# Performance work log

Hardware: AMD Instinct MI355X
Metric: run time of the kernel (lower is better)

The kernel has to match this reference:

```python
import jax, jax.numpy as jnp
import numpy as np

N = 8192  # number of DAG nodes


def setup_inputs() -> dict:
    key = jax.random.key(0)
    k1, k2, k3 = jax.random.split(key, 3)
    thresholds = jax.random.normal(k1, (N,), dtype=jnp.float32)
    # children in [-1, N): -1 marks a leaf (no child)
    left = jax.random.randint(k2, (N,), -1, N, dtype=jnp.int32)
    right = jax.random.randint(k3, (N,), -1, N, dtype=jnp.int32)
    return {"thresholds": thresholds, "left": left, "right": right}


def reference(thresholds, left, right):
    # BFS fixed-point reachability from node 0, N sequential relaxation steps.
    n_nodes = left.shape[0]

    def step(reachable, _):
        # route children of reachable non-leaf nodes into a scatter; dump
        # inactive slots into the sentinel index n_nodes (dropped on slice)
        active_left = jnp.where(reachable & (left >= 0), left, n_nodes)
        active_right = jnp.where(reachable & (right >= 0), right, n_nodes)
        new_reachable = jnp.zeros(n_nodes + 1, dtype=jnp.bool_)
        new_reachable = new_reachable.at[active_left].set(True)
        new_reachable = new_reachable.at[active_right].set(True)
        new_reachable = new_reachable.at[0].set(True)
        return (new_reachable[:n_nodes] | reachable, None)

    init = jnp.zeros(n_nodes, dtype=jnp.bool_).at[0].set(True)
    mask, _ = jax.lax.scan(step, init, None, length=n_nodes)
    return mask
```

## Files before the change

kernel.cpp:

```cpp
#include <hip/hip_runtime.h>


#define NMAX 8192
#define BLK  256

__global__ __launch_bounds__(BLK) void dag_reach_kernel(
    const int* __restrict__ left,
    const int* __restrict__ right,
    int* __restrict__ out,
    int n)
{
    __shared__ int2         sLR[NMAX];
    __shared__ unsigned int visited[NMAX / 32];
    __shared__ int          frontier[NMAX];
    __shared__ int          s_qcount;

    const int tid = threadIdx.x;

    {
        const int4* l4 = (const int4*)left;
        const int4* r4 = (const int4*)right;
        const int nv = n / 4;
        for (int i = tid; i < nv; i += BLK) {
            int4 l = l4[i];
            int4 r = r4[i];
            int b = i * 4;
            sLR[b + 0] = make_int2(l.x, r.x);
            sLR[b + 1] = make_int2(l.y, r.y);
            sLR[b + 2] = make_int2(l.z, r.z);
            sLR[b + 3] = make_int2(l.w, r.w);
        }
    }
    for (int i = tid; i < NMAX / 32; i += BLK) visited[i] = 0u;
    if (tid == 0) { visited[0] = 1u; frontier[0] = 0; s_qcount = 1; }
    __syncthreads();

    int start = 0, end = 1;
    while (start < end) {
        for (int i = start + tid; i < end; i += BLK) {
            int node = frontier[i];
            int2 lr = sLR[node];
            if (lr.x >= 0) {
                unsigned int bit = 1u << (lr.x & 31);
                unsigned int old = atomicOr(&visited[lr.x >> 5], bit);
                if (!(old & bit))
                    frontier[atomicAdd(&s_qcount, 1)] = lr.x;
            }
            if (lr.y >= 0) {
                unsigned int bit = 1u << (lr.y & 31);
                unsigned int old = atomicOr(&visited[lr.y >> 5], bit);
                if (!(old & bit))
                    frontier[atomicAdd(&s_qcount, 1)] = lr.y;
            }
        }
        __syncthreads();
        start = end;
        end = s_qcount;
        __syncthreads();
    }

    {
        int4* o4 = (int4*)out;
        const int nv = n / 4;
        for (int i = tid; i < nv; i += BLK) {
            unsigned int w = visited[i >> 3];
            int sh = (i & 7) * 4;
            o4[i] = make_int4((int)((w >> (sh + 0)) & 1u),
                              (int)((w >> (sh + 1)) & 1u),
                              (int)((w >> (sh + 2)) & 1u),
                              (int)((w >> (sh + 3)) & 1u));
        }
    }
}

extern "C" void kernel_launch(void* const* d_in, const int* in_sizes, int n_in,
                              void* d_out, int out_size, void* d_ws, size_t ws_size,
                              hipStream_t stream)
{
    const int* left  = (const int*)d_in[1];
    const int* right = (const int*)d_in[2];
    int* out = (int*)d_out;
    const int n = in_sizes[1];

    dag_reach_kernel<<<1, BLK, 0, stream>>>(left, right, out, n);
}
```

Before: 74.42 us.

## Replace level-synchronous BFS with asynchronous work-queue traversal

Replaces the per-level BFS loop, which needs two block-wide barriers per level, with an asynchronous shared-memory work queue. Each of 256 worker threads claims a queue slot, spins until a node is written there, expands its children and claims the next slot. Termination is detected when the count of processed nodes equals the count of reserved slots. The block grows to 1024 threads for loading and output while only 256 do the traversal. This removes the barrier cost on long, narrow BFS chains, but it adds volatile polling, extra atomics, and a risk of spin or livelock behaviour across wavefronts.

After: 77.52 us. 4.2% more time.

```diff
diff --git a/kernel.cpp b/kernel.cpp
--- a/kernel.cpp
+++ b/kernel.cpp
@@ -1,8 +1,9 @@
 #include <hip/hip_runtime.h>
 
 
-#define NMAX 8192
-#define BLK  256
+#define NMAX  8192
+#define BLK   1024
+#define NWORK 256
 
 __global__ __launch_bounds__(BLK) void dag_reach_kernel(
     const int* __restrict__ left,
@@ -12,15 +13,15 @@
 {
     __shared__ int2         sLR[NMAX];
     __shared__ unsigned int visited[NMAX / 32];
-    __shared__ int          frontier[NMAX];
-    __shared__ int          s_qcount;
+    __shared__ int          queue[NMAX];
+    __shared__ int          s_tail, s_res, s_done;
 
     const int tid = threadIdx.x;
+    const int nv = n / 4;
 
     {
         const int4* l4 = (const int4*)left;
         const int4* r4 = (const int4*)right;
-        const int nv = n / 4;
         for (int i = tid; i < nv; i += BLK) {
             int4 l = l4[i];
             int4 r = r4[i];
@@ -31,37 +32,57 @@
             sLR[b + 3] = make_int2(l.w, r.w);
         }
     }
+    for (int i = tid; i < NMAX; i += BLK) queue[i] = -1;
     for (int i = tid; i < NMAX / 32; i += BLK) visited[i] = 0u;
-    if (tid == 0) { visited[0] = 1u; frontier[0] = 0; s_qcount = 1; }
+    if (tid == 0) { s_tail = 0; s_res = 1; s_done = 0; queue[0] = 0; visited[0] = 1u; }
     __syncthreads();
 
-    int start = 0, end = 1;
-    while (start < end) {
-        for (int i = start + tid; i < end; i += BLK) {
-            int node = frontier[i];
-            int2 lr = sLR[node];
-            if (lr.x >= 0) {
-                unsigned int bit = 1u << (lr.x & 31);
-                unsigned int old = atomicOr(&visited[lr.x >> 5], bit);
-                if (!(old & bit))
-                    frontier[atomicAdd(&s_qcount, 1)] = lr.x;
-            }
-            if (lr.y >= 0) {
-                unsigned int bit = 1u << (lr.y & 31);
-                unsigned int old = atomicOr(&visited[lr.y >> 5], bit);
-                if (!(old & bit))
-                    frontier[atomicAdd(&s_qcount, 1)] = lr.y;
+    if (tid < NWORK) {
+        volatile int* vq    = queue;
+        volatile int* vdone = &s_done;
+        volatile int* vres  = &s_res;
+
+        int myidx = atomicAdd(&s_tail, 1);
+        int node  = -1;
+
+        for (;;) {
+            if (node < 0 && myidx < NMAX) node = vq[myidx];
+            bool ready = (node >= 0);
+            if (__any(ready)) {
+                if (ready) {
+                    int2 lr = sLR[node];
+                    if (lr.x >= 0) {
+                        unsigned int bit = 1u << (lr.x & 31);
+                        unsigned int old = atomicOr(&visited[lr.x >> 5], bit);
+                        if (!(old & bit)) {
+                            int s = atomicAdd(&s_res, 1);
+                            queue[s] = lr.x;
+                        }
+                    }
+                    if (lr.y >= 0) {
+                        unsigned int bit = 1u << (lr.y & 31);
+                        unsigned int old = atomicOr(&visited[lr.y >> 5], bit);
+                        if (!(old & bit)) {
+                            int s = atomicAdd(&s_res, 1);
+                            queue[s] = lr.y;
+                        }
+                    }
+                    __threadfence_block();
+                    atomicAdd(&s_done, 1);
+                    myidx = atomicAdd(&s_tail, 1);
+                    node  = -1;
+                }
+            } else {
+                int d = *vdone;
+                int r = *vres;
+                if (d == r) break;
             }
         }
-        __syncthreads();
-        start = end;
-        end = s_qcount;
-        __syncthreads();
     }
+    __syncthreads();
 
     {
         int4* o4 = (int4*)out;
-        const int nv = n / 4;
         for (int i = tid; i < nv; i += BLK) {
             unsigned int w = visited[i >> 3];
             int sh = (i & 7) * 4;
```

## Replace level-synchronous BFS queue with asynchronous bitmap-owner propagation

Applied to the files above, without the earlier changes.

The frontier queue and per-level barriers are replaced by an owner-computes scheme. Each of 1024 threads owns 8 nodes and spins on a volatile read of the shared visited bitmap, expanding newly set bits with atomicOr. Convergence is found by quiescence counters and then a verification pass with block barriers, which avoids one barrier pair per BFS level along long chains. The risks are wasted spinning, heavy atomic contention on shared words, and correctness that depends on the quiescence heuristic plus the verify loop.

New measurement: 72.32 us. 2.8% less time.

```diff
diff --git a/kernel.cpp b/kernel.cpp
--- a/kernel.cpp
+++ b/kernel.cpp
@@ -2,7 +2,7 @@
 
 
 #define NMAX 8192
-#define BLK  256
+#define BLK  1024
 
 __global__ __launch_bounds__(BLK) void dag_reach_kernel(
     const int* __restrict__ left,
@@ -12,15 +12,14 @@
 {
     __shared__ int2         sLR[NMAX];
     __shared__ unsigned int visited[NMAX / 32];
-    __shared__ int          frontier[NMAX];
-    __shared__ int          s_qcount;
+    __shared__ int          flag[2];
 
     const int tid = threadIdx.x;
+    const int nv  = n / 4;
 
     {
         const int4* l4 = (const int4*)left;
         const int4* r4 = (const int4*)right;
-        const int nv = n / 4;
         for (int i = tid; i < nv; i += BLK) {
             int4 l = l4[i];
             int4 r = r4[i];
@@ -32,43 +31,81 @@
         }
     }
     for (int i = tid; i < NMAX / 32; i += BLK) visited[i] = 0u;
-    if (tid == 0) { visited[0] = 1u; frontier[0] = 0; s_qcount = 1; }
+    if (tid == 0) { visited[0] = 1u; flag[0] = 0; flag[1] = 0; }
     __syncthreads();
 
-    int start = 0, end = 1;
-    while (start < end) {
-        for (int i = start + tid; i < end; i += BLK) {
-            int node = frontier[i];
-            int2 lr = sLR[node];
-            if (lr.x >= 0) {
-                unsigned int bit = 1u << (lr.x & 31);
-                unsigned int old = atomicOr(&visited[lr.x >> 5], bit);
-                if (!(old & bit))
-                    frontier[atomicAdd(&s_qcount, 1)] = lr.x;
-            }
-            if (lr.y >= 0) {
-                unsigned int bit = 1u << (lr.y & 31);
-                unsigned int old = atomicOr(&visited[lr.y >> 5], bit);
-                if (!(old & bit))
-                    frontier[atomicAdd(&s_qcount, 1)] = lr.y;
+    const int wi   = tid >> 2;
+    const int sh   = (tid & 3) * 8;
+    const int base = tid * 8;
+    unsigned int expd = 0u;
+    unsigned int verified = 0u;
+    volatile unsigned int* vvis = visited;
+
+    for (int round = 0; ; ++round) {
+        {
+            const int K = (round == 0) ? 32 : 8;
+            int quiet = 0;
+            while (quiet < K) {
+                unsigned int byte = (vvis[wi] >> sh) & 0xFFu;
+                unsigned int pend = byte & ~expd;
+                if (pend) {
+                    expd |= pend;
+                    do {
+                        int b = __ffs(pend) - 1;
+                        pend &= pend - 1;
+                        int2 lr = sLR[base + b];
+                        if (lr.x >= 0) atomicOr(&visited[lr.x >> 5], 1u << (lr.x & 31));
+                        if (lr.y >= 0) atomicOr(&visited[lr.y >> 5], 1u << (lr.y & 31));
+                        pend = pend;
+                    } while (pend);
+                    quiet = 0;
+                } else {
+                    quiet = __any(0) ? 0 : quiet + 1;
+                }
+                if (__any((vvis[wi] >> sh) & ~expd & 0xFFu)) quiet = 0;
             }
         }
         __syncthreads();
-        start = end;
-        end = s_qcount;
+
+        bool bad = false;
+        {
+            unsigned int byte = (visited[wi] >> sh) & 0xFFu;
+            expd |= byte;
+            unsigned int chk = expd & ~verified;
+            while (chk) {
+                int b = __ffs(chk) - 1;
+                chk &= chk - 1;
+                int2 lr = sLR[base + b];
+                if (lr.x >= 0) {
+                    unsigned int bit = 1u << (lr.x & 31);
+                    unsigned int old = atomicOr(&visited[lr.x >> 5], bit);
+                    if (!(old & bit)) bad = true;
+                }
+                if (lr.y >= 0) {
+                    unsigned int bit = 1u << (lr.y & 31);
+                    unsigned int old = atomicOr(&visited[lr.y >> 5], bit);
+                    if (!(old & bit)) bad = true;
+                }
+            }
+            verified = expd;
+        }
+        if (bad)      flag[round & 1] = 1;
+        if (tid == 0) flag[(round + 1) & 1] = 0;
         __syncthreads();
+        int f = flag[round & 1];
+        __syncthreads();
+        if (!f) break;
     }
 
     {
         int4* o4 = (int4*)out;
-        const int nv = n / 4;
         for (int i = tid; i < nv; i += BLK) {
             unsigned int w = visited[i >> 3];
-            int sh = (i & 7) * 4;
-            o4[i] = make_int4((int)((w >> (sh + 0)) & 1u),
-                              (int)((w >> (sh + 1)) & 1u),
-                              (int)((w >> (sh + 2)) & 1u),
-                              (int)((w >> (sh + 3)) & 1u));
+            int s = (i & 7) * 4;
+            o4[i] = make_int4((int)((w >> (s + 0)) & 1u),
+                              (int)((w >> (s + 1)) & 1u),
+                              (int)((w >> (s + 2)) & 1u),
+                              (int)((w >> (s + 3)) & 1u));
         }
     }
 }
```
